# Optimization experiments

Hardware: AMD Instinct MI355X
Metric: run time of the kernel (lower is better)

## Reference

```python
import jax, jax.numpy as jnp
import numpy as np

H = 16       # num_attention_heads
HKV = 4      # num_key_value_heads
D = 128      # head_dim
CHUNK = 64   # input_chunk_size
RBS = 64     # retrieval_block_size


def setup_inputs() -> dict:
    key = jax.random.key(0)
    ks = jax.random.split(key, 9)
    B, S, HID = 1, 2048, 2048
    RLEN = 2048  # retrieval_block_num * RBS = (S // CHUNK) * RBS
    inv = 0.02
    return {
        "hidden_states": jax.random.normal(ks[0], (B, S, HID), jnp.float32),
        "cos": jax.random.uniform(ks[1], (B, S, D), jnp.float32),
        "sin": jax.random.uniform(ks[2], (B, S, D), jnp.float32),
        "retrieval_k": jax.random.normal(ks[3], (B, HKV, RLEN, D), jnp.float32),
        "retrieval_v": jax.random.normal(ks[4], (B, HKV, RLEN, D), jnp.float32),
        "Wq": jax.random.normal(ks[5], (HID, H * D), jnp.float32) * inv,
        "Wk": jax.random.normal(ks[6], (HID, HKV * D), jnp.float32) * inv,
        "Wv": jax.random.normal(ks[7], (HID, HKV * D), jnp.float32) * inv,
        "Wo": jax.random.normal(ks[8], (H * D, HID), jnp.float32) * inv,
    }


def _rope(x, cos, sin):
    # x: [B, h, S, D]; cos/sin: [B, S, D] (HF apply_rotary_pos_emb, unsqueeze head dim)
    c = cos[:, None, :, :]
    s = sin[:, None, :, :]
    x1, x2 = jnp.split(x, 2, axis=-1)
    rot = jnp.concatenate([-x2, x1], axis=-1)
    return x * c + rot * s


def reference(hidden_states, cos, sin, retrieval_k, retrieval_v, Wq, Wk, Wv, Wo):
    B, S, HID = hidden_states.shape
    G = H // HKV
    scale = D ** -0.5

    q = (hidden_states @ Wq).reshape(B, S, H, D).transpose(0, 2, 1, 3)    # [B,H,S,D]
    k = (hidden_states @ Wk).reshape(B, S, HKV, D).transpose(0, 2, 1, 3)  # [B,HKV,S,D]
    v = (hidden_states @ Wv).reshape(B, S, HKV, D).transpose(0, 2, 1, 3)

    q = _rope(q, cos, sin)
    k = _rope(k, cos, sin)

    # GQA: expand kv heads
    k_full = jnp.repeat(k, G, axis=1)  # [B,H,S,D]
    v_full = jnp.repeat(v, G, axis=1)

    # ---- causal part over input keys ----
    s1 = jnp.einsum('bhqd,bhkd->bhqk', q, k_full) * scale
    causal = jnp.tril(jnp.ones((S, S), bool))
    s1 = jnp.where(causal[None, None], s1, -jnp.inf)

    # ---- retrieval part: chunk c attends retrieval block (c-1) only ----
    C = S // CHUNK
    R = retrieval_k.shape[2] // RBS
    rK = retrieval_k.reshape(B, HKV, R, RBS, D)
    rV = retrieval_v.reshape(B, HKV, R, RBS, D)
    blk_idx = jnp.clip(jnp.arange(C) - 1, 0, R - 1)          # chunk 0 masked below
    rK_sel = jnp.repeat(rK[:, :, blk_idx], G, axis=1)        # [B,H,C,RBS,D]
    rV_sel = jnp.repeat(rV[:, :, blk_idx], G, axis=1)
    qc = q.reshape(B, H, C, CHUNK, D)
    s2 = jnp.einsum('bhcqd,bhckd->bhcqk', qc, rK_sel) * scale
    valid = (jnp.arange(C) >= 1)[None, None, :, None, None]
    s2 = jnp.where(valid, s2, -jnp.inf)

    # ---- joint (numerically stable) softmax over causal + retrieval keys ----
    m1 = jnp.max(s1, axis=-1)                                # [B,H,S]
    m2 = jnp.max(s2, axis=-1).reshape(B, H, S)               # -inf for chunk 0
    m = jnp.maximum(m1, m2)
    e1 = jnp.exp(s1 - m[..., None])
    e2 = jnp.exp(s2 - m.reshape(B, H, C, CHUNK)[..., None])
    denom = e1.sum(-1) + e2.sum(-1).reshape(B, H, S)         # [B,H,S]
    o1 = jnp.einsum('bhqk,bhkd->bhqd', e1, v_full)
    o2 = jnp.einsum('bhcqk,bhckd->bhcqd', e2, rV_sel).reshape(B, H, S, D)
    attn = (o1 + o2) / denom[..., None]                      # [B,H,S,D]

    out = attn.transpose(0, 2, 1, 3).reshape(B, S, H * D)
    return out @ Wo
```

## Files before the change

### kernel.cpp

```cpp
#include <hip/hip_runtime.h>
#include <stdint.h>

#define H_    16
#define HKV_  4
#define D_    128
#define S_    2048
#define HID_  2048
#define RLEN_ 2048

typedef unsigned short u16;
typedef __attribute__((ext_vector_type(4))) float f32x4;
typedef __attribute__((ext_vector_type(16))) float f32x16;
typedef __attribute__((ext_vector_type(8))) __bf16 bf16x8;
typedef __attribute__((ext_vector_type(4))) unsigned short u16x4;
typedef __attribute__((ext_vector_type(8))) unsigned short u16x8;
typedef __attribute__((ext_vector_type(2))) unsigned int u32x2;

__device__ __forceinline__ u16 f2bf(float f) {
  union { float f; unsigned u; } v; v.f = f;
  unsigned r = v.u + 0x7FFFu + ((v.u >> 16) & 1u);
  return (u16)(r >> 16);
}
__device__ __forceinline__ float bf2f(u16 h) {
  union { unsigned u; float f; } v; v.u = ((unsigned)h) << 16;
  return v.f;
}
__device__ __forceinline__ float exp2v(float x) {
  float r; asm("v_exp_f32 %0, %1" : "=v"(r) : "v"(x)); return r;
}
__device__ __forceinline__ unsigned cvtpk(float lo, float hi) {
  unsigned r; asm("v_cvt_pk_bf16_f32 %0, %1, %2" : "=v"(r) : "v"(lo), "v"(hi)); return r;
}
__device__ __forceinline__ void pl32swap(unsigned &a, unsigned &b) {
  u32x2 r = __builtin_amdgcn_permlane32_swap(a, b, false, false);
  a = r.x; b = r.y;
}
__device__ __forceinline__ float xhalf_max(float v) {
  unsigned a = __float_as_uint(v), b = a;
  pl32swap(a, b);
  return fmaxf(__uint_as_float(a), __uint_as_float(b));
}
__device__ __forceinline__ float xhalf_add(float v) {
  unsigned a = __float_as_uint(v), b = a;
  pl32swap(a, b);
  return __uint_as_float(a) + __uint_as_float(b);
}
__device__ __forceinline__ void drain_then_sync() {
  asm volatile("s_waitcnt vmcnt(0) lgkmcnt(0)" ::: "memory");
  __syncthreads();
}
__device__ __forceinline__ void drain4_then_sync() {
  asm volatile("s_waitcnt vmcnt(4) lgkmcnt(0)" ::: "memory");
  __syncthreads();
}

#define GLL(srcp, ldsp) \
  __builtin_amdgcn_global_load_lds((const __attribute__((address_space(1))) unsigned int*)(srcp), \
                                   (__attribute__((address_space(3))) unsigned int*)(ldsp), 16, 0, 0)

__global__ void k_cvt(const float* __restrict__ in, u16* __restrict__ out, int n4) {
  int i = blockIdx.x * 256 + threadIdx.x;
  if (i >= n4) return;
  float4 v = ((const float4*)in)[i];
  u16x4 o;
  o.x = f2bf(v.x); o.y = f2bf(v.y); o.z = f2bf(v.z); o.w = f2bf(v.w);
  ((u16x4*)out)[i] = o;
}

__global__ void k_transw_qkv(const float* __restrict__ Wq, const float* __restrict__ Wk,
                             const float* __restrict__ Wv, u16* __restrict__ wtq) {
  __shared__ float tile[32][33];
  const int bid = blockIdx.x;
  const float* in; u16* out; int N, bx, by;
  if (bid < 4096)      { in = Wq; out = wtq;                          N = 2048; bx = (bid & 63) * 32;        by = (bid >> 6) * 32; }
  else if (bid < 5120) { in = Wk; out = wtq + (size_t)2048 * 2048;    N = 512;  bx = ((bid - 4096) & 15) * 32; by = ((bid - 4096) >> 4) * 32; }
  else                 { in = Wv; out = wtq + (size_t)2560 * 2048;    N = 512;  bx = ((bid - 5120) & 15) * 32; by = ((bid - 5120) >> 4) * 32; }
  const int K = 2048;
  int tx = threadIdx.x, ty = threadIdx.y;
#pragma unroll
  for (int i = 0; i < 32; i += 8)
    tile[ty + i][tx] = in[(size_t)(by + ty + i) * N + bx + tx];
  __syncthreads();
#pragma unroll
  for (int i = 0; i < 32; i += 8)
    out[(size_t)(bx + ty + i) * K + by + tx] = f2bf(tile[tx][ty + i]);
}

__global__ void k_transw(const float* __restrict__ in, u16* __restrict__ out, int K, int N) {
  __shared__ float tile[32][33];
  int bx = blockIdx.x * 32, by = blockIdx.y * 32;
  int tx = threadIdx.x, ty = threadIdx.y;
#pragma unroll
  for (int i = 0; i < 32; i += 8)
    tile[ty + i][tx] = in[(size_t)(by + ty + i) * N + bx + tx];
  __syncthreads();
#pragma unroll
  for (int i = 0; i < 32; i += 8)
    out[(size_t)(bx + ty + i) * K + by + tx] = f2bf(tile[tx][ty + i]);
}

__global__ __launch_bounds__(256) void k_gemm(const u16* __restrict__ A, const u16* __restrict__ Bt,
                                              u16* __restrict__ Cb, int M, int N, int K,
                                              int Kpart, int Krem) {
  __shared__ __attribute__((aligned(16))) u16 As[3][128 * 32];
  __shared__ __attribute__((aligned(16))) u16 Bs[3][128 * 32];
  const int bm = blockIdx.y * 128, bn = blockIdx.x * 128;
  const int kz0 = blockIdx.z * Kpart;
  const int kz1 = kz0 + Kpart + ((blockIdx.z == gridDim.z - 1) ? Krem : 0);
  const int nsteps = (kz1 - kz0) >> 5;
  u16* C = Cb + (size_t)blockIdx.z * M * N;
  const int tid = threadIdx.x, wave = tid >> 6, lane = tid & 63;
  const int wr = wave >> 1, wc = wave & 1;
  const int l15 = lane & 15, lhi = lane >> 4;
  const int so = wave * 512;
  f32x4 acc[4][4] = {};
  const int cw = ((tid & 3) ^ ((tid >> 3) & 3)) * 8;
  const u16* pA  = A  + (size_t)(bm + (tid >> 2)) * K + cw;
  const u16* pA2 = A  + (size_t)(bm + 64 + (tid >> 2)) * K + cw;
  const u16* pB  = Bt + (size_t)(bn + (tid >> 2)) * K + cw;
  const u16* pB2 = Bt + (size_t)(bn + 64 + (tid >> 2)) * K + cw;
  const int sc = (lhi ^ ((l15 >> 1) & 3)) * 8;

  auto stage = [&](int s, int buf) {
    const int k0 = kz0 + s * 32;
    GLL(pA + k0,  &As[buf][so]);
    GLL(pA2 + k0, &As[buf][2048 + so]);
    GLL(pB + k0,  &Bs[buf][so]);
    GLL(pB2 + k0, &Bs[buf][2048 + so]);
  };

  stage(0, 0);
  if (nsteps > 1) { stage(1, 1); drain4_then_sync(); }
  else            { drain_then_sync(); }

  for (int s = 0; s < nsteps; s++) {
    const int buf = s % 3;
    const bool deep = (s + 2 < nsteps);
    if (deep) stage(s + 2, (s + 2) % 3);
    bf16x8 af[4], bfr[4];
#pragma unroll
    for (int m = 0; m < 4; m++)
      af[m] = *(const bf16x8*)(&As[buf][(wr * 64 + m * 16 + l15) * 32 + sc]);
#pragma unroll
    for (int n = 0; n < 4; n++)
      bfr[n] = *(const bf16x8*)(&Bs[buf][(wc * 64 + n * 16 + l15) * 32 + sc]);
#pragma unroll
    for (int m = 0; m < 4; m++)
#pragma unroll
      for (int n = 0; n < 4; n++)
        acc[m][n] = __builtin_amdgcn_mfma_f32_16x16x32_bf16(af[m], bfr[n], acc[m][n], 0, 0, 0);
    if (deep) drain4_then_sync();
    else      drain_then_sync();
  }
  const int r0 = bm + wr * 64, c0 = bn + wc * 64;
#pragma unroll
  for (int m = 0; m < 4; m++)
#pragma unroll
    for (int n = 0; n < 4; n++) {
      int r = r0 + m * 16 + lhi * 4, cc = c0 + n * 16 + l15;
#pragma unroll
      for (int j = 0; j < 4; j++)
        C[(size_t)(r + j) * N + cc] = f2bf(acc[m][n][j]);
    }
}

__global__ void k_comb2(const u16* __restrict__ c0, const u16* __restrict__ c1,
                        float* __restrict__ out, int n8) {
  int i = blockIdx.x * 256 + threadIdx.x;
  if (i >= n8) return;
  u16x8 a = ((const u16x8*)c0)[i];
  u16x8 b = ((const u16x8*)c1)[i];
  float4 o0, o1;
  o0.x = bf2f(a[0]) + bf2f(b[0]); o0.y = bf2f(a[1]) + bf2f(b[1]);
  o0.z = bf2f(a[2]) + bf2f(b[2]); o0.w = bf2f(a[3]) + bf2f(b[3]);
  o1.x = bf2f(a[4]) + bf2f(b[4]); o1.y = bf2f(a[5]) + bf2f(b[5]);
  o1.z = bf2f(a[6]) + bf2f(b[6]); o1.w = bf2f(a[7]) + bf2f(b[7]);
  ((float4*)out)[i * 2]     = o0;
  ((float4*)out)[i * 2 + 1] = o1;
}

__global__ void k_ropeq(const u16* __restrict__ qp0, const float* __restrict__ cs,
                        const float* __restrict__ sn, u16* __restrict__ Q) {
  const u16* qp1 = qp0 + (size_t)2048 * 3072;
  int tid = threadIdx.x;
  int idx = blockIdx.x * 4 + (tid >> 6);
  int d = tid & 63;
  int h = idx >> 11, s = idx & (S_ - 1);
  size_t base = (size_t)s * 3072 + h * 128;
  float x1 = bf2f(qp0[base + d])      + bf2f(qp1[base + d]);
  float x2 = bf2f(qp0[base + d + 64]) + bf2f(qp1[base + d + 64]);
  float c1 = cs[s * D_ + d], s1v = sn[s * D_ + d];
  float c2 = cs[s * D_ + d + 64], s2v = sn[s * D_ + d + 64];
  const float sc = 0.12751744422f;
  u16* o = Q + ((size_t)h * S_ + s) * D_;
  o[d]      = f2bf((x1 * c1 - x2 * s1v) * sc);
  o[d + 64] = f2bf((x2 * c2 + x1 * s2v) * sc);
}

__global__ void k_ropekv(const u16* __restrict__ qp0, const float* __restrict__ cs,
                         const float* __restrict__ sn, u16* __restrict__ Ksw,
                         u16* __restrict__ Vts) {
  const u16* qp1 = qp0 + (size_t)2048 * 3072;
  int tid = threadIdx.x;
  int idx = blockIdx.x * 4 + (tid >> 6);
  int d = tid & 63;
  int kv = idx >> 11, s = idx & (S_ - 1);
  size_t kb = (size_t)s * 3072 + 2048 + kv * 128;
  size_t vb = kb + 512;
  float x1 = bf2f(qp0[kb + d])      + bf2f(qp1[kb + d]);
  float x2 = bf2f(qp0[kb + d + 64]) + bf2f(qp1[kb + d + 64]);
  float v1 = bf2f(qp0[vb + d])      + bf2f(qp1[vb + d]);
  float v2 = bf2f(qp0[vb + d + 64]) + bf2f(qp1[vb + d + 64]);
  float c1 = cs[s * D_ + d], s1v = sn[s * D_ + d];
  float c2 = cs[s * D_ + d + 64], s2v = sn[s * D_ + d + 64];
  u16* ko = Ksw + ((size_t)kv * S_ + s) * D_;
  int sw = (s & 7) << 3;
  ko[d ^ sw]        = f2bf(x1 * c1 - x2 * s1v);
  ko[(d + 64) ^ sw] = f2bf(x2 * c2 + x1 * s2v);
  u16* vo = Vts + (size_t)kv * D_ * S_;
  int sc64 = s & ~63, sl = s & 63;
  vo[(size_t)d * S_        + sc64 + (sl ^ ((d & 7) << 3))]        = f2bf(v1);
  vo[(size_t)(d + 64) * S_ + sc64 + (sl ^ (((d + 64) & 7) << 3))] = f2bf(v2);
}

__global__ void k_retr(const float* __restrict__ rk, const float* __restrict__ rv,
                       u16* __restrict__ Krs, u16* __restrict__ Vtrs) {
  int tid = threadIdx.x;
  int idx = blockIdx.x * 2 + (tid >> 7);
  int d = tid & 127;
  int kv = idx >> 11, r = idx & (RLEN_ - 1);
  size_t base = ((size_t)kv * RLEN_ + r) * D_;
  Krs[base + (d ^ ((r & 7) << 3))] = f2bf(rk[base + d]);
  int rc = r & ~63, rl = r & 63;
  Vtrs[((size_t)kv * D_ + d) * RLEN_ + rc + (rl ^ ((d & 7) << 3))] = f2bf(rv[base + d]);
}

__global__ __launch_bounds__(256, 3) void k_attn(
    const u16* __restrict__ Q, const u16* __restrict__ Ksw, const u16* __restrict__ Vts,
    const u16* __restrict__ Krs, const u16* __restrict__ Vtrs,
    u16* __restrict__ Opart, float* __restrict__ Ml) {
  __shared__ __attribute__((aligned(16))) char smem[49152];
  u16* Kl = (u16*)smem;
  u16* Vl = (u16*)(smem + 16384);

  const int e = 83 - blockIdx.x, kvh = blockIdx.y, qs = blockIdx.z;
  int c, part, np;
  if (e < 7)       { c = e;               part = 0;           np = 1; }
  else if (e < 23) { c = 7 + ((e - 7) >> 1);  part = (e - 7) & 1;  np = 2; }
  else if (e < 47) { c = 15 + (e - 23) / 3;   part = (e - 23) % 3; np = 3; }
  else if (e < 79) { c = 23 + ((e - 47) >> 2); part = (e - 47) & 3; np = 4; }
  else             { c = 31;              part = e - 79;      np = 5; }
  const int nt = (c == 0) ? 1 : (c + 2);
  const int t0 = (part * nt) / np, t1 = ((part + 1) * nt) / np;

  const int tid = threadIdx.x, wave = tid >> 6, lane = tid & 63;
  const int h = kvh * 4 + wave;
  const int bp = h * 84 + e;
  const int l31 = lane & 31, hf = lane >> 5;
  const int qrow = c * 64 + qs * 32 + l31;

  bf16x8 qf[8];
  {
    const u16* qp = Q + ((size_t)h * S_ + qrow) * D_ + hf * 8;
#pragma unroll
    for (int m = 0; m < 8; m++) qf[m] = *(const bf16x8*)(qp + m * 16);
  }
  float mq = -1e30f, lq = 0.f;
  f32x16 accO[4] = {};

  const int kgo = (tid >> 4) * 128 + (tid & 15) * 8;
  const int vgo = (tid >> 3) * 2048 + (tid & 7) * 8;
  u16* const kdst = Kl + wave * 512;

  const int cm1 = (c >= 1) ? (c - 1) : 0;
  const u16* krb = Krs + (size_t)kvh * RLEN_ * D_ + (size_t)cm1 * 64 * D_;
  const u16* vrb = Vtrs + (size_t)kvh * D_ * RLEN_ + cm1 * 64;
  const u16* kst = Ksw + (size_t)kvh * S_ * D_ + (size_t)t0 * 64 * D_;
  const u16* vst = Vts + (size_t)kvh * D_ * S_ + t0 * 64;
  int ts = t0;

#pragma unroll
  for (int p = 0; p < 4; p++) GLL(kst + p * 2048 + kgo, kdst + p * 2048);
#pragma unroll
  for (int p = 0; p < 4; p++) GLL(vst + p * 65536 + vgo, Vl + wave * 512 + p * 2048);
  ts = t0 + 1;
  if (ts == c + 1) { kst = krb; vst = vrb; } else { kst += 64 * D_; vst += 64; }
  drain_then_sync();

  for (int t = t0; t < t1; t++) {
    const int vb = (t - t0) & 1;
    const bool pf = (t + 1 < t1);
    f32x16 sacc[2] = {};
    {
      const char* Kbuf = (const char*)Kl;
#pragma unroll
      for (int kb = 0; kb < 2; kb++)
#pragma unroll
        for (int m = 0; m < 8; m++) {
          int by = ((kb * 32 + l31) << 8) + ((m * 32 + hf * 16) ^ ((l31 & 7) << 4));
          bf16x8 kf = *(const bf16x8*)(Kbuf + by);
          sacc[kb] = __builtin_amdgcn_mfma_f32_32x32x16_bf16(kf, qf[m], sacc[kb], 0, 0, 0);
        }
    }
    drain_then_sync();
    if (pf) {
#pragma unroll
      for (int p = 0; p < 4; p++) GLL(kst + p * 2048 + kgo, kdst + p * 2048);
      u16* vd = Vl + (vb ^ 1) * 8192 + wave * 512;
#pragma unroll
      for (int p = 0; p < 4; p++) GLL(vst + p * 65536 + vgo, vd + p * 2048);
      ts++;
      if (ts == c + 1) { kst = krb; vst = vrb; } else { kst += 64 * D_; vst += 64; }
    }
    if (t == c) {
#pragma unroll
      for (int kb = 0; kb < 2; kb++) {
        const int koffm = kb * 32 - qs * 32;
#pragma unroll
        for (int r = 0; r < 16; r++) {
          int kloc = (r & 3) + 8 * (r >> 2) + 4 * hf + koffm;
          if (kloc > l31) sacc[kb][r] = -1e30f;
        }
      }
    }
    float tmax = sacc[0][0];
#pragma unroll
    for (int r = 1; r < 16; r++) tmax = fmaxf(tmax, sacc[0][r]);
#pragma unroll
    for (int r = 0; r < 16; r++) tmax = fmaxf(tmax, sacc[1][r]);
    tmax = xhalf_max(tmax);
    if (!__all(tmax - mq <= 11.5f)) {
      float mn = fmaxf(mq, tmax);
      float f = exp2v(mq - mn);
      mq = mn; lq *= f;
#pragma unroll
      for (int dt = 0; dt < 4; dt++)
#pragma unroll
        for (int r = 0; r < 16; r++) accO[dt][r] *= f;
    }
    float ps = 0.f;
#pragma unroll
    for (int kb = 0; kb < 2; kb++)
#pragma unroll
      for (int r = 0; r < 16; r++) {
        float p = exp2v(sacc[kb][r] - mq);
        sacc[kb][r] = p; ps += p;
      }
    lq += xhalf_add(ps);
    unsigned W[2][8];
#pragma unroll
    for (int kb = 0; kb < 2; kb++)
#pragma unroll
      for (int g = 0; g < 4; g++) {
        W[kb][2 * g]     = cvtpk(sacc[kb][4 * g],     sacc[kb][4 * g + 1]);
        W[kb][2 * g + 1] = cvtpk(sacc[kb][4 * g + 2], sacc[kb][4 * g + 3]);
      }
    const char* Vbuf = (const char*)(Vl + vb * 8192);
    __builtin_amdgcn_s_setprio(1);
#pragma unroll
    for (int kb = 0; kb < 2; kb++)
#pragma unroll
      for (int st = 0; st < 2; st++) {
        unsigned x0 = W[kb][4 * st], y0 = W[kb][4 * st + 2];
        unsigned x1 = W[kb][4 * st + 1], y1 = W[kb][4 * st + 3];
        pl32swap(x0, y0);
        pl32swap(x1, y1);
        union { unsigned u[4]; bf16x8 v; } pfr;
        pfr.u[0] = x0; pfr.u[1] = x1; pfr.u[2] = y0; pfr.u[3] = y1;
#pragma unroll
        for (int dt = 0; dt < 4; dt++) {
          int vby = ((dt * 32 + l31) << 7) +
                    ((kb * 64 + st * 32 + hf * 16) ^ ((l31 & 7) << 4));
          bf16x8 vf = *(const bf16x8*)(Vbuf + vby);
          accO[dt] = __builtin_amdgcn_mfma_f32_32x32x16_bf16(vf, pfr.v, accO[dt], 0, 0, 0);
        }
      }
    __builtin_amdgcn_s_setprio(0);
    if (pf) drain4_then_sync();
  }

  u16* op = Opart + (size_t)bp * 8192 + (size_t)(qs * 32 + l31) * 128;
#pragma unroll
  for (int dt = 0; dt < 4; dt++)
#pragma unroll
    for (int j = 0; j < 4; j++) {
      u16x4 o;
#pragma unroll
      for (int b = 0; b < 4; b++) o[b] = f2bf(accO[dt][4 * j + b]);
      *(u16x4*)(op + dt * 32 + j * 8 + hf * 4) = o;
    }
  if (hf == 0) {
    Ml[(size_t)bp * 128 + qs * 32 + l31]      = mq;
    Ml[(size_t)bp * 128 + 64 + qs * 32 + l31] = lq;
  }
}

__global__ __launch_bounds__(256) void k_combine(const u16* __restrict__ Opart,
                                                 const float* __restrict__ Ml,
                                                 u16* __restrict__ attn) {
  const int c = blockIdx.x, h = blockIdx.y;
  const int t = threadIdx.x;
  const int q = t >> 2, d0 = (t & 3) * 32;
  int base, np;
  if (c < 7)       { base = c;                 np = 1; }
  else if (c < 15) { base = 7 + 2 * (c - 7);   np = 2; }
  else if (c < 23) { base = 23 + 3 * (c - 15); np = 3; }
  else if (c < 31) { base = 47 + 4 * (c - 23); np = 4; }
  else             { base = 79;                np = 5; }
  const size_t pb = (size_t)h * 84 + base;

  float m = -1e30f;
  for (int p = 0; p < np; p++) m = fmaxf(m, Ml[(pb + p) * 128 + q]);
  float l = 0.f;
  float N[32];
#pragma unroll
  for (int i = 0; i < 32; i++) N[i] = 0.f;
  for (int p = 0; p < np; p++) {
    const float mp = Ml[(pb + p) * 128 + q];
    const float lp = Ml[(pb + p) * 128 + 64 + q];
    const float w = exp2v(mp - m);
    l += w * lp;
    const u16* op = Opart + (pb + p) * 8192 + q * 128 + d0;
#pragma unroll
    for (int i = 0; i < 4; i++) {
      u16x8 v = ((const u16x8*)op)[i];
#pragma unroll
      for (int ee = 0; ee < 8; ee++) N[i * 8 + ee] += w * bf2f(v[ee]);
    }
  }
  const float inv = 1.f / l;
  u16* dst = attn + (size_t)(c * 64 + q) * (H_ * D_) + h * 128 + d0;
#pragma unroll
  for (int i = 0; i < 4; i++) {
    u16x8 o;
#pragma unroll
    for (int ee = 0; ee < 8; ee++) o[ee] = f2bf(N[i * 8 + ee] * inv);
    ((u16x8*)dst)[i] = o;
  }
}

extern "C" void kernel_launch(void* const* d_in, const int* in_sizes, int n_in,
                              void* d_out, int out_size, void* d_ws, size_t ws_size,
                              hipStream_t stream) {
  const float* hs = (const float*)d_in[0];
  const float* cs = (const float*)d_in[1];
  const float* sn = (const float*)d_in[2];
  const float* rk = (const float*)d_in[3];
  const float* rv = (const float*)d_in[4];
  const float* Wq = (const float*)d_in[5];
  const float* Wk = (const float*)d_in[6];
  const float* Wv = (const float*)d_in[7];
  const float* Wo = (const float*)d_in[8];
  float* out = (float*)d_out;
  char* ws = (char*)d_ws;
  if (ws_size < (size_t)(56u << 20)) return;

  u16* hsb  = (u16*)(ws);
  u16* wtq  = (u16*)(ws + (8u << 20));
  u16* qkvP = (u16*)(ws + (20u << 20));
  u16* Qr   = (u16*)(ws + (44u << 20));
  u16* Ks   = (u16*)(ws + (52u << 20));
  u16* Vts  = (u16*)(ws + (54u << 20));
  u16* Krs  = (u16*)(ws + (8u << 20));
  u16* Vtrs = (u16*)(ws + (10u << 20));
  u16* wto  = (u16*)(ws + (12u << 20));
  u16* Opart= (u16*)(ws + (20u << 20));
  float* Ml = (float*)(ws + (41u << 20));
  u16* attn = (u16*)(ws);
  u16* Cp   = (u16*)(ws + (20u << 20));

  dim3 tb(32, 8);
  k_cvt<<<4096, 256, 0, stream>>>(hs, hsb, 1048576);
  k_transw_qkv<<<6144, tb, 0, stream>>>(Wq, Wk, Wv, wtq);
  k_gemm<<<dim3(24, 16, 2), 256, 0, stream>>>(hsb, wtq, qkvP, 2048, 3072, 2048, 1024, 0);
  k_ropeq<<<8192, 256, 0, stream>>>(qkvP, cs, sn, Qr);
  k_ropekv<<<2048, 256, 0, stream>>>(qkvP, cs, sn, Ks, Vts);
  k_retr<<<4096, 256, 0, stream>>>(rk, rv, Krs, Vtrs);
  k_transw<<<dim3(64, 64), tb, 0, stream>>>(Wo, wto, 2048, 2048);
  k_attn<<<dim3(84, 4, 2), 256, 0, stream>>>(Qr, Ks, Vts, Krs, Vtrs, Opart, Ml);
  k_combine<<<dim3(32, 16), 256, 0, stream>>>(Opart, Ml, attn);
  k_gemm<<<dim3(16, 16, 2), 256, 0, stream>>>(attn, wto, Cp, 2048, 2048, 2048, 1024, 0);
  k_comb2<<<2048, 256, 0, stream>>>(Cp, Cp + (size_t)2048 * 2048, out, 524288);
}
```

Before: 159.0 us.

## Use 256x128 GEMM tiles with deeper split-K and rearrange workspace

The GEMM tile grows from 128x128 to 256x128 per block, so each wave now computes 128x64 with 32 accumulators, which raises arithmetic intensity per LDS load. Split-K goes to 3 for the QKV projection and 4 for the output projection to keep enough blocks on the device, and the rope and combine kernels now sum 3 and 4 partial buffers. Workspace offsets are reshuffled so the extra partials fit. The risks are higher register pressure under launch_bounds(256,2), extra partial-sum traffic, and bf16 rounding on more partials.

New measurement: 176.6 us. +11.0%, slower.

```diff
diff --git a/kernel.cpp b/kernel.cpp
--- a/kernel.cpp
+++ b/kernel.cpp
@@ -51,6 +51,10 @@
 }
 __device__ __forceinline__ void drain4_then_sync() {
   asm volatile("s_waitcnt vmcnt(4) lgkmcnt(0)" ::: "memory");
+  __syncthreads();
+}
+__device__ __forceinline__ void drain6_then_sync() {
+  asm volatile("s_waitcnt vmcnt(6) lgkmcnt(0)" ::: "memory");
   __syncthreads();
 }
 
@@ -99,62 +103,66 @@
     out[(size_t)(bx + ty + i) * K + by + tx] = f2bf(tile[tx][ty + i]);
 }
 
-__global__ __launch_bounds__(256) void k_gemm(const u16* __restrict__ A, const u16* __restrict__ Bt,
-                                              u16* __restrict__ Cb, int M, int N, int K,
-                                              int Kpart, int Krem) {
-  __shared__ __attribute__((aligned(16))) u16 As[3][128 * 32];
+__global__ __launch_bounds__(256, 2) void k_gemm(const u16* __restrict__ A, const u16* __restrict__ Bt,
+                                                 u16* __restrict__ Cb, int M, int N, int K,
+                                                 int Kpart, int Krem) {
+  __shared__ __attribute__((aligned(16))) u16 As[3][256 * 32];
   __shared__ __attribute__((aligned(16))) u16 Bs[3][128 * 32];
-  const int bm = blockIdx.y * 128, bn = blockIdx.x * 128;
+  const int bm = blockIdx.y * 256, bn = blockIdx.x * 128;
   const int kz0 = blockIdx.z * Kpart;
   const int kz1 = kz0 + Kpart + ((blockIdx.z == gridDim.z - 1) ? Krem : 0);
   const int nsteps = (kz1 - kz0) >> 5;
   u16* C = Cb + (size_t)blockIdx.z * M * N;
   const int tid = threadIdx.x, wave = tid >> 6, lane = tid & 63;
-  const int wr = wave >> 1, wc = wave & 1;
+  const int wrM = wave >> 1, wcN = wave & 1;
   const int l15 = lane & 15, lhi = lane >> 4;
   const int so = wave * 512;
-  f32x4 acc[4][4] = {};
+  f32x4 acc[8][4] = {};
   const int cw = ((tid & 3) ^ ((tid >> 3) & 3)) * 8;
-  const u16* pA  = A  + (size_t)(bm + (tid >> 2)) * K + cw;
-  const u16* pA2 = A  + (size_t)(bm + 64 + (tid >> 2)) * K + cw;
-  const u16* pB  = Bt + (size_t)(bn + (tid >> 2)) * K + cw;
-  const u16* pB2 = Bt + (size_t)(bn + 64 + (tid >> 2)) * K + cw;
+  const u16* pA0 = A + (size_t)(bm + (tid >> 2)) * K + cw;
+  const u16* pA1 = A + (size_t)(bm + 64 + (tid >> 2)) * K + cw;
+  const u16* pA2 = A + (size_t)(bm + 128 + (tid >> 2)) * K + cw;
+  const u16* pA3 = A + (size_t)(bm + 192 + (tid >> 2)) * K + cw;
+  const u16* pB0 = Bt + (size_t)(bn + (tid >> 2)) * K + cw;
+  const u16* pB1 = Bt + (size_t)(bn + 64 + (tid >> 2)) * K + cw;
   const int sc = (lhi ^ ((l15 >> 1) & 3)) * 8;
 
   auto stage = [&](int s, int buf) {
     const int k0 = kz0 + s * 32;
-    GLL(pA + k0,  &As[buf][so]);
-    GLL(pA2 + k0, &As[buf][2048 + so]);
-    GLL(pB + k0,  &Bs[buf][so]);
-    GLL(pB2 + k0, &Bs[buf][2048 + so]);
+    GLL(pA0 + k0, &As[buf][so]);
+    GLL(pA1 + k0, &As[buf][2048 + so]);
+    GLL(pA2 + k0, &As[buf][4096 + so]);
+    GLL(pA3 + k0, &As[buf][6144 + so]);
+    GLL(pB0 + k0, &Bs[buf][so]);
+    GLL(pB1 + k0, &Bs[buf][2048 + so]);
   };
 
   stage(0, 0);
-  if (nsteps > 1) { stage(1, 1); drain4_then_sync(); }
+  if (nsteps > 1) { stage(1, 1); drain6_then_sync(); }
   else            { drain_then_sync(); }
 
   for (int s = 0; s < nsteps; s++) {
     const int buf = s % 3;
     const bool deep = (s + 2 < nsteps);
     if (deep) stage(s + 2, (s + 2) % 3);
-    bf16x8 af[4], bfr[4];
-#pragma unroll
-    for (int m = 0; m < 4; m++)
-      af[m] = *(const bf16x8*)(&As[buf][(wr * 64 + m * 16 + l15) * 32 + sc]);
+    bf16x8 af[8], bfr[4];
+#pragma unroll
+    for (int m = 0; m < 8; m++)
+      af[m] = *(const bf16x8*)(&As[buf][(wrM * 128 + m * 16 + l15) * 32 + sc]);
 #pragma unroll
     for (int n = 0; n < 4; n++)
-      bfr[n] = *(const bf16x8*)(&Bs[buf][(wc * 64 + n * 16 + l15) * 32 + sc]);
-#pragma unroll
-    for (int m = 0; m < 4; m++)
+      bfr[n] = *(const bf16x8*)(&Bs[buf][(wcN * 64 + n * 16 + l15) * 32 + sc]);
+#pragma unroll
+    for (int m = 0; m < 8; m++)
 #pragma unroll
       for (int n = 0; n < 4; n++)
         acc[m][n] = __builtin_amdgcn_mfma_f32_16x16x32_bf16(af[m], bfr[n], acc[m][n], 0, 0, 0);
-    if (deep) drain4_then_sync();
+    if (deep) drain6_then_sync();
     else      drain_then_sync();
   }
-  const int r0 = bm + wr * 64, c0 = bn + wc * 64;
-#pragma unroll
-  for (int m = 0; m < 4; m++)
+  const int r0 = bm + wrM * 128, c0 = bn + wcN * 64;
+#pragma unroll
+  for (int m = 0; m < 8; m++)
 #pragma unroll
     for (int n = 0; n < 4; n++) {
       int r = r0 + m * 16 + lhi * 4, cc = c0 + n * 16 + l15;
@@ -164,17 +172,23 @@
     }
 }
 
-__global__ void k_comb2(const u16* __restrict__ c0, const u16* __restrict__ c1,
-                        float* __restrict__ out, int n8) {
+__global__ void k_comb4(const u16* __restrict__ c0, float* __restrict__ out, int n8) {
   int i = blockIdx.x * 256 + threadIdx.x;
   if (i >= n8) return;
+  const size_t zs = (size_t)2048 * 2048 / 8;
   u16x8 a = ((const u16x8*)c0)[i];
-  u16x8 b = ((const u16x8*)c1)[i];
+  u16x8 b = ((const u16x8*)c0)[i + zs];
+  u16x8 cc = ((const u16x8*)c0)[i + 2 * zs];
+  u16x8 d = ((const u16x8*)c0)[i + 3 * zs];
   float4 o0, o1;
-  o0.x = bf2f(a[0]) + bf2f(b[0]); o0.y = bf2f(a[1]) + bf2f(b[1]);
-  o0.z = bf2f(a[2]) + bf2f(b[2]); o0.w = bf2f(a[3]) + bf2f(b[3]);
-  o1.x = bf2f(a[4]) + bf2f(b[4]); o1.y = bf2f(a[5]) + bf2f(b[5]);
-  o1.z = bf2f(a[6]) + bf2f(b[6]); o1.w = bf2f(a[7]) + bf2f(b[7]);
+  o0.x = (bf2f(a[0]) + bf2f(b[0])) + (bf2f(cc[0]) + bf2f(d[0]));
+  o0.y = (bf2f(a[1]) + bf2f(b[1])) + (bf2f(cc[1]) + bf2f(d[1]));
+  o0.z = (bf2f(a[2]) + bf2f(b[2])) + (bf2f(cc[2]) + bf2f(d[2]));
+  o0.w = (bf2f(a[3]) + bf2f(b[3])) + (bf2f(cc[3]) + bf2f(d[3]));
+  o1.x = (bf2f(a[4]) + bf2f(b[4])) + (bf2f(cc[4]) + bf2f(d[4]));
+  o1.y = (bf2f(a[5]) + bf2f(b[5])) + (bf2f(cc[5]) + bf2f(d[5]));
+  o1.z = (bf2f(a[6]) + bf2f(b[6])) + (bf2f(cc[6]) + bf2f(d[6]));
+  o1.w = (bf2f(a[7]) + bf2f(b[7])) + (bf2f(cc[7]) + bf2f(d[7]));
   ((float4*)out)[i * 2]     = o0;
   ((float4*)out)[i * 2 + 1] = o1;
 }
@@ -182,13 +196,14 @@
 __global__ void k_ropeq(const u16* __restrict__ qp0, const float* __restrict__ cs,
                         const float* __restrict__ sn, u16* __restrict__ Q) {
   const u16* qp1 = qp0 + (size_t)2048 * 3072;
+  const u16* qp2 = qp0 + (size_t)2 * 2048 * 3072;
   int tid = threadIdx.x;
   int idx = blockIdx.x * 4 + (tid >> 6);
   int d = tid & 63;
   int h = idx >> 11, s = idx & (S_ - 1);
   size_t base = (size_t)s * 3072 + h * 128;
-  float x1 = bf2f(qp0[base + d])      + bf2f(qp1[base + d]);
-  float x2 = bf2f(qp0[base + d + 64]) + bf2f(qp1[base + d + 64]);
+  float x1 = bf2f(qp0[base + d]) + bf2f(qp1[base + d]) + bf2f(qp2[base + d]);
+  float x2 = bf2f(qp0[base + d + 64]) + bf2f(qp1[base + d + 64]) + bf2f(qp2[base + d + 64]);
   float c1 = cs[s * D_ + d], s1v = sn[s * D_ + d];
   float c2 = cs[s * D_ + d + 64], s2v = sn[s * D_ + d + 64];
   const float sc = 0.12751744422f;
@@ -201,16 +216,17 @@
                          const float* __restrict__ sn, u16* __restrict__ Ksw,
                          u16* __restrict__ Vts) {
   const u16* qp1 = qp0 + (size_t)2048 * 3072;
+  const u16* qp2 = qp0 + (size_t)2 * 2048 * 3072;
   int tid = threadIdx.x;
   int idx = blockIdx.x * 4 + (tid >> 6);
   int d = tid & 63;
   int kv = idx >> 11, s = idx & (S_ - 1);
   size_t kb = (size_t)s * 3072 + 2048 + kv * 128;
   size_t vb = kb + 512;
-  float x1 = bf2f(qp0[kb + d])      + bf2f(qp1[kb + d]);
-  float x2 = bf2f(qp0[kb + d + 64]) + bf2f(qp1[kb + d + 64]);
-  float v1 = bf2f(qp0[vb + d])      + bf2f(qp1[vb + d]);
-  float v2 = bf2f(qp0[vb + d + 64]) + bf2f(qp1[vb + d + 64]);
+  float x1 = bf2f(qp0[kb + d]) + bf2f(qp1[kb + d]) + bf2f(qp2[kb + d]);
+  float x2 = bf2f(qp0[kb + d + 64]) + bf2f(qp1[kb + d + 64]) + bf2f(qp2[kb + d + 64]);
+  float v1 = bf2f(qp0[vb + d]) + bf2f(qp1[vb + d]) + bf2f(qp2[vb + d]);
+  float v2 = bf2f(qp0[vb + d + 64]) + bf2f(qp1[vb + d + 64]) + bf2f(qp2[vb + d + 64]);
   float c1 = cs[s * D_ + d], s1v = sn[s * D_ + d];
   float c2 = cs[s * D_ + d + 64], s2v = sn[s * D_ + d + 64];
   u16* ko = Ksw + ((size_t)kv * S_ + s) * D_;
@@ -458,27 +474,27 @@
   u16* hsb  = (u16*)(ws);
   u16* wtq  = (u16*)(ws + (8u << 20));
   u16* qkvP = (u16*)(ws + (20u << 20));
-  u16* Qr   = (u16*)(ws + (44u << 20));
-  u16* Ks   = (u16*)(ws + (52u << 20));
-  u16* Vts  = (u16*)(ws + (54u << 20));
-  u16* Krs  = (u16*)(ws + (8u << 20));
-  u16* Vtrs = (u16*)(ws + (10u << 20));
-  u16* wto  = (u16*)(ws + (12u << 20));
-  u16* Opart= (u16*)(ws + (20u << 20));
-  float* Ml = (float*)(ws + (41u << 20));
+  u16* Qr   = (u16*)(ws);
+  u16* Ks   = (u16*)(ws + (8u << 20));
+  u16* Vts  = (u16*)(ws + (10u << 20));
+  u16* Krs  = (u16*)(ws + (12u << 20));
+  u16* Vtrs = (u16*)(ws + (14u << 20));
+  u16* wto  = (u16*)(ws + (16u << 20));
+  u16* Opart= (u16*)(ws + (24u << 20));
+  float* Ml = (float*)(ws + (45u << 20));
   u16* attn = (u16*)(ws);
-  u16* Cp   = (u16*)(ws + (20u << 20));
+  u16* Cp   = (u16*)(ws + (24u << 20));
 
   dim3 tb(32, 8);
   k_cvt<<<4096, 256, 0, stream>>>(hs, hsb, 1048576);
   k_transw_qkv<<<6144, tb, 0, stream>>>(Wq, Wk, Wv, wtq);
-  k_gemm<<<dim3(24, 16, 2), 256, 0, stream>>>(hsb, wtq, qkvP, 2048, 3072, 2048, 1024, 0);
+  k_gemm<<<dim3(24, 8, 3), 256, 0, stream>>>(hsb, wtq, qkvP, 2048, 3072, 2048, 672, 32);
   k_ropeq<<<8192, 256, 0, stream>>>(qkvP, cs, sn, Qr);
   k_ropekv<<<2048, 256, 0, stream>>>(qkvP, cs, sn, Ks, Vts);
   k_retr<<<4096, 256, 0, stream>>>(rk, rv, Krs, Vtrs);
   k_transw<<<dim3(64, 64), tb, 0, stream>>>(Wo, wto, 2048, 2048);
   k_attn<<<dim3(84, 4, 2), 256, 0, stream>>>(Qr, Ks, Vts, Krs, Vtrs, Opart, Ml);
   k_combine<<<dim3(32, 16), 256, 0, stream>>>(Opart, Ml, attn);
-  k_gemm<<<dim3(16, 16, 2), 256, 0, stream>>>(attn, wto, Cp, 2048, 2048, 2048, 1024, 0);
-  k_comb2<<<2048, 256, 0, stream>>>(Cp, Cp + (size_t)2048 * 2048, out, 524288);
-}
+  k_gemm<<<dim3(16, 8, 4), 256, 0, stream>>>(attn, wto, Cp, 2048, 2048, 2048, 512, 0);
+  k_comb4<<<2048, 256, 0, stream>>>(Cp, out, 524288);
+}
```
